# Performance work log

Hardware: AMD Instinct MI355X
Metric: run time of the kernel (lower is better)

Reference implementation:

```python
import jax, jax.numpy as jnp
import numpy as np


def _ln(z, g, b):
    m = z.mean(-1, keepdims=True)
    v = ((z - m) ** 2).mean(-1, keepdims=True)
    return (z - m) * jax.lax.rsqrt(v + 1e-5) * g + b


def _pe(T, D):
    # standard sinusoidal positional encoding (T, D)
    pos = np.arange(T)[:, None]
    i = np.arange(D // 2)[None, :]
    ang = pos / np.power(10000.0, 2.0 * i / D)
    pe = np.zeros((T, D), dtype=np.float32)
    pe[:, 0::2] = np.sin(ang)
    pe[:, 1::2] = np.cos(ang)
    return jnp.asarray(pe)


def _whconv(z, Hinc, filt, W, b):
    # Wavelet hypergraph convolution: psi diag(filt) psi^{-1} Z W + b
    # psi = heat-kernel wavelet of normalized hypergraph Laplacian, 2nd-order Taylor (K=2, s=1)
    S = Hinc.shape[0]
    Dv = Hinc.sum(1) + 1e-6          # node degrees
    De = Hinc.sum(0) + 1e-6          # hyperedge degrees
    Hn = Hinc * (Dv ** -0.5)[:, None]
    A = (Hn / De[None, :]) @ Hn.T    # Dv^-1/2 H De^-1 H^T Dv^-1/2
    I = jnp.eye(S, dtype=z.dtype)
    L = I - A
    L2 = 0.5 * (L @ L)
    psi = I - L + L2                  # exp(-L) approx
    psi_inv = I + L + L2              # exp(+L) approx
    return psi @ (filt[:, None] * (psi_inv @ z)) @ W + b


def setup_inputs():
    S, T, F, D, NS, E, K = 2048, 64, 16, 256, 4, 128, 32
    key = jax.random.key(0)
    ks = iter(jax.random.split(key, 64))
    nrm = lambda shp: jax.random.normal(next(ks), shp, jnp.float32) * 0.02
    return dict(
        x=jax.random.normal(next(ks), (S, T, F), jnp.float32),
        snapshot=(jax.random.uniform(next(ks), (NS, S, E)) < 0.05).astype(jnp.float32),
        params_snapshot=jax.random.uniform(next(ks), (NS,), jnp.float32, 0.0, 0.99),
        beta=jnp.array([0.33, 0.33, 0.33], jnp.float32),
        W_emb=nrm((F, D)), b_emb=jnp.zeros((D,), jnp.float32),
        Wq=nrm((D, D)), bq=jnp.zeros((D,), jnp.float32),
        Wk=nrm((D, D)), bk=jnp.zeros((D,), jnp.float32),
        Wv=nrm((D, D)), bv=jnp.zeros((D,), jnp.float32),
        Wo=nrm((D, D)), bo=jnp.zeros((D,), jnp.float32),
        ln1_g=jnp.ones((D,), jnp.float32), ln1_b=jnp.zeros((D,), jnp.float32),
        W_int=nrm((D, D)), b_int=jnp.zeros((D,), jnp.float32),
        W_mix=nrm((2 * D, D)), b_mix=jnp.zeros((D,), jnp.float32),
        ln2_g=jnp.ones((D,), jnp.float32), ln2_b=jnp.zeros((D,), jnp.float32),
        Wt=nrm((D, D)), bt=jnp.zeros((D,), jnp.float32), vt=nrm((D,)),
        Wh1=nrm((D, D)), bh1=jnp.zeros((D,), jnp.float32), filt1=jnp.ones((S,), jnp.float32),
        Wh2=nrm((D, D)), bh2=jnp.zeros((D,), jnp.float32), filt2=jnp.ones((S,), jnp.float32),
        Wa=nrm((D, D)), Wb=nrm((D, D)), Wg=nrm((D, D)), bg=jnp.zeros((D,), jnp.float32),
        Wm1=nrm((D, D)), bm1=jnp.zeros((D,), jnp.float32),
        Wm2=nrm((D, 1)), bm2=jnp.zeros((1,), jnp.float32),
        num_edges=K,
    )


def reference(x, snapshot, params_snapshot, beta, W_emb, b_emb, Wq, bq, Wk, bk, Wv, bv,
              Wo, bo, ln1_g, ln1_b, W_int, b_int, W_mix, b_mix, ln2_g, ln2_b,
              Wt, bt, vt, Wh1, bh1, filt1, Wh2, bh2, filt2, Wa, Wb, Wg, bg,
              Wm1, bm1, Wm2, bm2, num_edges):
    S, T, _ = x.shape
    D = W_emb.shape[1]
    H = 8
    dh = D // H
    # feature embedding + positional encoding
    h = x @ W_emb + b_emb + _pe(T, D)
    # intra-stock (per-stock temporal) multi-head self-attention + residual + LN
    q = (h @ Wq + bq).reshape(S, T, H, dh)
    k = (h @ Wk + bk).reshape(S, T, H, dh)
    v = (h @ Wv + bv).reshape(S, T, H, dh)
    att = jax.nn.softmax(jnp.einsum('sqhd,skhd->shqk', q, k) / jnp.sqrt(jnp.float32(dh)), axis=-1)
    o = jnp.einsum('shqk,skhd->sqhd', att, v).reshape(S, T, D) @ Wo + bo
    h = _ln(h + o, ln1_g, ln1_b)
    # intensity function + mixing layer (Linear -> ReLU -> LayerNorm)
    intensity = jax.nn.softplus(h @ W_int + b_int)
    z = jax.nn.relu(jnp.concatenate([h, intensity], axis=-1) @ W_mix + b_mix)
    h = _ln(z, ln2_g, ln2_b)
    # temporal attention pooling: (S,T,D) -> (S,D)
    u = jnp.tanh(h @ Wt + bt)
    a = jax.nn.softmax(u @ vt, axis=-1)          # (S,T)
    xs = jnp.einsum('st,std->sd', a, h)           # (S,D)
    # per-snapshot two-layer wavelet hypergraph conv (dropout = eval identity)
    def per_snap(Hinc):
        r1 = jax.nn.leaky_relu(_whconv(xs, Hinc, filt1, Wh1, bh1), 0.1)
        return _whconv(r1, Hinc, filt2, Wh2, bh2)
    reps = jax.vmap(per_snap)(snapshot)           # (NS,S,D)
    hyper = jnp.einsum('n,nsd->sd', params_snapshot, reps)
    # dynamic graph learning: top-k learned similarity graph
    sim = (xs @ Wa) @ (xs @ Wb).T / jnp.sqrt(jnp.float32(D))
    kth = jax.lax.top_k(sim, num_edges)[0][:, -1]
    Adyn = jax.nn.softmax(jnp.where(sim >= kth[:, None], sim, -jnp.inf), axis=-1)
    dyn = jax.nn.relu(Adyn @ xs @ Wg + bg)
    # fusion ('sum' mode) + MLP head
    w = jax.nn.softmax(beta)
    fused = w[0] * xs + w[1] * dyn + w[2] * hyper
    return jax.nn.relu(fused @ Wm1 + bm1) @ Wm2 + bm2   # (S,1)
```

## Files before the change

### kernel.cpp

```cpp
#include <hip/hip_runtime.h>
#include <math.h>

#define S_ 2048
#define T_ 64
#define F_ 16
#define D_ 256
#define NS_ 4
#define E_ 128
#define H_ 8
#define SD_ (S_*D_)
#define PS 264

#define PK_ATT 0
#define PK_WO  393216
#define PK_WI  524288
#define PK_WT  655360
#define PK_WM  786432
#define PKBASE 11674112

typedef __attribute__((ext_vector_type(8))) short bf16x8;
typedef __attribute__((ext_vector_type(4))) float f32x4;

__device__ __forceinline__ float warp_sum64(float v){
  #pragma unroll
  for (int o=32;o>=1;o>>=1) v += __shfl_xor(v,o);
  return v;
}
__device__ __forceinline__ float warp_max64(float v){
  #pragma unroll
  for (int o=32;o>=1;o>>=1) v = fmaxf(v,__shfl_xor(v,o));
  return v;
}
__device__ __forceinline__ float softplus_f(float v){
  return fmaxf(v,0.f) + log1pf(__expf(-fabsf(v)));
}
__device__ __forceinline__ float tanh_f(float v){
  float t = __expf(-2.f*fabsf(v));
  float r = (1.f-t)/(1.f+t);
  return copysignf(r, v);
}
__device__ __forceinline__ void splitf(float f, short& h, short& l){
  unsigned u = __float_as_uint(f);
  unsigned hb = (u + 0x7FFFu + ((u>>16)&1u)) >> 16;
  float fl = f - __uint_as_float(hb<<16);
  unsigned v = __float_as_uint(fl);
  unsigned lb = (v + 0x7FFFu + ((v>>16)&1u)) >> 16;
  h = (short)hb; l = (short)lb;
}
__device__ __forceinline__ f32x4 mfma3(bf16x8 ah, bf16x8 al, bf16x8 bh, bf16x8 bl, f32x4 c){
  c = __builtin_amdgcn_mfma_f32_16x16x32_bf16(al, bh, c, 0,0,0);
  c = __builtin_amdgcn_mfma_f32_16x16x32_bf16(ah, bl, c, 0,0,0);
  c = __builtin_amdgcn_mfma_f32_16x16x32_bf16(ah, bh, c, 0,0,0);
  return c;
}
__device__ __forceinline__ void afrag_f32(const float* base, int stride, int rbase, int ks, int lane, bf16x8& hi, bf16x8& lo){
  const float* p = base + (rbase + (lane&15))*stride + ks + ((lane>>4)<<3);
  #pragma unroll
  for (int jj=0;jj<8;++jj){ short h,l; splitf(p[jj],h,l); hi[jj]=h; lo[jj]=l; }
}
__device__ __forceinline__ bf16x8 afrag_pk(const short* plane, int rbase, int ks, int lane){
  return *(const bf16x8*)(plane + (rbase + (lane&15))*PS + ks + ((lane>>4)<<3));
}
__device__ __forceinline__ void bfrag_pk(const unsigned* pk, int tile, int lane, bf16x8& hi, bf16x8& lo){
  const unsigned* p = pk + (((tile<<6) + lane)<<3);
  #pragma unroll
  for (int jj=0;jj<8;++jj){ unsigned u=p[jj]; hi[jj]=(short)(u & 0xffffu); lo[jj]=(short)(u>>16); }
}
__device__ __forceinline__ void store_h(short* Hh, short* Hl, int r, int c, float f){
  short h,l; splitf(f,h,l);
  Hh[r*PS+c]=h; Hl[r*PS+c]=l;
}
__device__ __forceinline__ float load_h(const short* Hh, const short* Hl, int r, int c){
  int idx=r*PS+c;
  return __uint_as_float(((unsigned)(unsigned short)Hh[idx])<<16)
       + __uint_as_float(((unsigned)(unsigned short)Hl[idx])<<16);
}

__global__ void pack_all(const float* __restrict__ Wq, const float* __restrict__ Wk,
                         const float* __restrict__ Wv, const float* __restrict__ Wo,
                         const float* __restrict__ Wint, const float* __restrict__ Wt,
                         const float* __restrict__ Wmix, short* __restrict__ pkc){
  int y = blockIdx.y;
  int i = blockIdx.x*256 + threadIdx.x;
  if (y < 3){
    const float* W = (y==0)?Wq:((y==1)?Wk:Wv);
    int jj=i&7, n=(i>>3)&15, q=(i>>7)&3, ntg=(i>>9)&15, kt=i>>13;
    float f = W[(kt*32 + q*8 + jj)*256 + (ntg*16+n)];
    short h,l; splitf(f,h,l);
    int hp = ntg>>2, ntl = ntg&3;
    int base = ((hp*8+kt)*6 + y*2)*2048;
    int local = ntl*512 + (q*16+n)*8 + jj;
    short* dst = pkc + PK_ATT;
    dst[base+local] = h;
    dst[base+2048+local] = l;
  } else {
    const float* W; short* dst; int ib = i;
    if (y==3){W=Wo;   dst=pkc+PK_WO;}
    else if (y==4){W=Wint; dst=pkc+PK_WI;}
    else if (y==5){W=Wt;   dst=pkc+PK_WT;}
    else if (y==6){W=Wmix; dst=pkc+PK_WM;}
    else          {W=Wmix; dst=pkc+PK_WM; ib = i + 65536;}
    int jj=ib&7, n=(ib>>3)&15, q=(ib>>7)&3, ntg=(ib>>9)&15, kt=ib>>13;
    float f = W[(kt*32 + q*8 + jj)*256 + (ntg*16+n)];
    short h,l; splitf(f,h,l);
    int dl = kt*16384 + ntg*512 + (q*16+n)*8 + jj;
    dst[dl] = h; dst[dl+8192] = l;
  }
}

__global__ void pe_kernel(float* __restrict__ pe){
  int i = blockIdx.x*256 + threadIdx.x;
  int t = i >> 8, d = i & 255;
  int ii = d >> 1;
  float w = __expf(-(float)ii * (logf(10000.f)/128.f));
  float ang = (float)t * w;
  pe[i] = (d & 1) ? cosf(ang) : sinf(ang);
}

__launch_bounds__(512,1)
__global__ void stageA_kernel(
    const float* __restrict__ x, const float* __restrict__ pe,
    const float* __restrict__ Wemb, const float* __restrict__ bemb,
    const float* __restrict__ bq, const float* __restrict__ bk, const float* __restrict__ bv,
    const float* __restrict__ bo,
    const float* __restrict__ ln1g, const float* __restrict__ ln1b,
    const float* __restrict__ bint,
    const float* __restrict__ bmix,
    const float* __restrict__ ln2g, const float* __restrict__ ln2b,
    const float* __restrict__ bt,
    const float* __restrict__ vt,
    const short* __restrict__ pkc,
    float* __restrict__ xs)
{
  __shared__ __attribute__((aligned(16))) short hbh[64*PS];
  __shared__ __attribute__((aligned(16))) short hbl[64*PS];
  __shared__ __attribute__((aligned(16))) char smem[85504];

  short*    wst   = (short*)smem;
  unsigned* k2f2  = (unsigned*)smem;
  unsigned* v2f2  = (unsigned*)(smem + 16384);
  float*    qb2   = (float*)(smem + 32768);
  float*    scb2  = (float*)(smem + 50176);
  float*    poolb = (float*)smem;

  const int j  = threadIdx.x;
  const int s  = blockIdx.x;
  const int w  = j >> 6;
  const int lane = j & 63;
  const int m_ = lane & 15, qd = lane >> 4;
  const int rg2 = w >> 1, par = w & 1;
  const int rbase = rg2*16;
  const int rv = w*8;
  const int c0 = lane;

  {
    float* xb = (float*)smem;
    const float* xp = x + (long)s*T_*F_;
    for (int i=j; i<T_*F_; i+=512) xb[i] = xp[i];
  }
  __syncthreads();

  {
    const float* xb = (const float*)smem;
    float acc[8][4];
    #pragma unroll
    for (int r=0;r<8;++r){acc[r][0]=0;acc[r][1]=0;acc[r][2]=0;acc[r][3]=0;}
    #pragma unroll
    for (int k=0;k<F_;++k){
      float w0=Wemb[k*D_+c0], w1=Wemb[k*D_+c0+64], w2=Wemb[k*D_+c0+128], w3=Wemb[k*D_+c0+192];
      #pragma unroll
      for (int r=0;r<8;++r){
        float hv = xb[(rv+r)*F_+k];
        acc[r][0]+=hv*w0; acc[r][1]+=hv*w1; acc[r][2]+=hv*w2; acc[r][3]+=hv*w3;
      }
    }
    float b0=bemb[c0],b1=bemb[c0+64],b2=bemb[c0+128],b3=bemb[c0+192];
    __syncthreads();
    #pragma unroll
    for (int r=0;r<8;++r){
      int t = rv+r;
      store_h(hbh,hbl,t,c0,     acc[r][0]+b0+pe[t*D_+c0]);
      store_h(hbh,hbl,t,c0+64,  acc[r][1]+b1+pe[t*D_+c0+64]);
      store_h(hbh,hbl,t,c0+128, acc[r][2]+b2+pe[t*D_+c0+128]);
      store_h(hbh,hbl,t,c0+192, acc[r][3]+b3+pe[t*D_+c0+192]);
    }
  }
  __syncthreads();

  bf16x8 AH[8], AL[8];
  #pragma unroll
  for (int kt=0;kt<8;++kt){
    AH[kt] = afrag_pk(hbh, rbase, kt*32, lane);
    AL[kt] = afrag_pk(hbl, rbase, kt*32, lane);
  }

  const float rs = 0.17677669529663687f;
  f32x4 co[8];
  #pragma unroll
  for (int t=0;t<8;++t) co[t] = (f32x4){0.f,0.f,0.f,0.f};

  for (int hp=0; hp<4; ++hp){
    f32x4 qa[2],ka[2],va[2];
    #pragma unroll
    for (int t=0;t<2;++t){
      qa[t]=(f32x4){0.f,0.f,0.f,0.f};
      ka[t]=(f32x4){0.f,0.f,0.f,0.f};
      va[t]=(f32x4){0.f,0.f,0.f,0.f};
    }
    bf16x8 pre[3];
    {
      const short* b0 = pkc + PK_ATT + (hp*8)*12288;
      #pragma unroll
      for (int r=0;r<3;++r) pre[r] = *(const bf16x8*)(b0 + (j+r*512)*8);
    }
    __syncthreads();
    for (int kt=0; kt<8; ++kt){
      short* wb = wst + (kt&1)*12288;
      #pragma unroll
      for (int r=0;r<3;++r) *(bf16x8*)(wb + (j+r*512)*8) = pre[r];
      __syncthreads();
      if (kt<7){
        const short* nb = pkc + PK_ATT + (hp*8+kt+1)*12288;
        #pragma unroll
        for (int r=0;r<3;++r) pre[r] = *(const bf16x8*)(nb + (j+r*512)*8);
      }
      bf16x8 ah = AH[kt], al = AL[kt];
      #pragma unroll
      for (int t=0;t<2;++t){
        int ntl = par*2+t;
        bf16x8 bh,bl;
        bh = *(bf16x8*)(wb +         ntl*512 + lane*8);
        bl = *(bf16x8*)(wb + 2048  + ntl*512 + lane*8);
        qa[t]=mfma3(ah,al,bh,bl,qa[t]);
        bh = *(bf16x8*)(wb + 4096  + ntl*512 + lane*8);
        bl = *(bf16x8*)(wb + 6144  + ntl*512 + lane*8);
        ka[t]=mfma3(ah,al,bh,bl,ka[t]);
        bh = *(bf16x8*)(wb + 8192  + ntl*512 + lane*8);
        bl = *(bf16x8*)(wb + 10240 + ntl*512 + lane*8);
        va[t]=mfma3(ah,al,bh,bl,va[t]);
      }
    }
    __syncthreads();
    #pragma unroll
    for (int t=0;t<2;++t){
      int ntg = par*2+t;
      #pragma unroll
      for (int r=0;r<4;++r){
        int trow = rbase + qd*4 + r;
        int pcp = ntg*16 + m_;
        int head = pcp >> 5;
        int cp = pcp & 31;
        int col = hp*64 + pcp;
        qb2[trow*68 + pcp] = (qa[t][r] + bq[col]) * rs;
        short hS,lS;
        float kv2 = ka[t][r] + bk[col];
        splitf(kv2,hS,lS);
        k2f2[head*2048 + (((trow>>4)*4 + (cp>>3))*16 + (trow&15))*8 + (cp&7)]
            = (unsigned)(unsigned short)hS | ((unsigned)(unsigned short)lS<<16);
        float vv2 = va[t][r] + bv[col];
        splitf(vv2,hS,lS);
        v2f2[head*2048 + ((((trow>>5)*2 + (cp>>4))*4 + ((trow>>3)&3))*16 + (cp&15))*8 + (trow&7)]
            = (unsigned)(unsigned short)hS | ((unsigned)(unsigned short)lS<<16);
      }
    }
    __syncthreads();
    float* scb = scb2 + par*4352;
    {
      bf16x8 ah,al;
      afrag_f32(qb2, 68, rbase, par*32, lane, ah, al);
      f32x4 sc4[4];
      #pragma unroll
      for (int nt=0;nt<4;++nt){
        bf16x8 bh,bl; bfrag_pk(k2f2 + par*2048, nt, lane, bh, bl);
        sc4[nt] = mfma3(ah,al,bh,bl,(f32x4){0.f,0.f,0.f,0.f});
      }
      #pragma unroll
      for (int r=0;r<4;++r){
        float mx = fmaxf(fmaxf(sc4[0][r],sc4[1][r]),fmaxf(sc4[2][r],sc4[3][r]));
        #pragma unroll
        for (int o=8;o>=1;o>>=1) mx = fmaxf(mx, __shfl_xor(mx,o));
        float es = 0.f;
        #pragma unroll
        for (int nt=0;nt<4;++nt){ float e=__expf(sc4[nt][r]-mx); sc4[nt][r]=e; es+=e; }
        #pragma unroll
        for (int o=8;o>=1;o>>=1) es += __shfl_xor(es,o);
        float inv = 1.f/es;
        int trow = rbase + qd*4 + r;
        #pragma unroll
        for (int nt=0;nt<4;++nt) scb[trow*68 + nt*16 + m_] = sc4[nt][r]*inv;
      }
    }
    {
      f32x4 oa[2];
      oa[0]=(f32x4){0.f,0.f,0.f,0.f}; oa[1]=(f32x4){0.f,0.f,0.f,0.f};
      #pragma unroll
      for (int kt=0;kt<2;++kt){
        bf16x8 ah2,al2; afrag_f32(scb, 68, rbase, kt*32, lane, ah2, al2);
        #pragma unroll
        for (int nt=0;nt<2;++nt){
          bf16x8 bh,bl; bfrag_pk(v2f2 + par*2048, kt*2+nt, lane, bh, bl);
          oa[nt]=mfma3(ah2,al2,bh,bl,oa[nt]);
        }
      }
      #pragma unroll
      for (int nt=0;nt<2;++nt){
        #pragma unroll
        for (int r=0;r<4;++r)
          qb2[(rbase+qd*4+r)*68 + par*32 + nt*16 + m_] = oa[nt][r];
      }
    }
    __syncthreads();
    for (int ks=0; ks<2; ++ks){
      bf16x8 ah,al; afrag_f32(qb2, 68, rbase, ks*32, lane, ah, al);
      const short* wob = pkc + PK_WO + (hp*2+ks)*16384 + lane*8;
      #pragma unroll
      for (int t=0;t<8;++t){
        int ntg = 2*t+par;
        bf16x8 bh = *(const bf16x8*)(wob + ntg*512);
        bf16x8 bl = *(const bf16x8*)(wob + 8192 + ntg*512);
        co[t]=mfma3(ah,al,bh,bl,co[t]);
      }
    }
  }

  #pragma unroll
  for (int t=0;t<8;++t){
    int cc = (2*t+par)*16+m_;
    float bov = bo[cc];
    #pragma unroll
    for (int r=0;r<4;++r){
      int row = rbase+qd*4+r;
      store_h(hbh,hbl,row,cc, load_h(hbh,hbl,row,cc) + co[t][r] + bov);
    }
  }
  __syncthreads();

  {
    float g0=ln1g[c0],g1=ln1g[c0+64],g2=ln1g[c0+128],g3=ln1g[c0+192];
    float bb0=ln1b[c0],bb1=ln1b[c0+64],bb2=ln1b[c0+128],bb3=ln1b[c0+192];
    for (int rr=0;rr<8;++rr){
      int t=rv+rr;
      float v0=load_h(hbh,hbl,t,c0),    v1=load_h(hbh,hbl,t,c0+64);
      float v2=load_h(hbh,hbl,t,c0+128),v3=load_h(hbh,hbl,t,c0+192);
      float sm=warp_sum64(v0+v1+v2+v3);
      float sq=warp_sum64(v0*v0+v1*v1+v2*v2+v3*v3);
      float mean=sm*(1.f/256.f);
      float inv=rsqrtf(fmaxf(sq*(1.f/256.f)-mean*mean,0.f)+1e-5f);
      store_h(hbh,hbl,t,c0,    (v0-mean)*inv*g0+bb0);
      store_h(hbh,hbl,t,c0+64, (v1-mean)*inv*g1+bb1);
      store_h(hbh,hbl,t,c0+128,(v2-mean)*inv*g2+bb2);
      store_h(hbh,hbl,t,c0+192,(v3-mean)*inv*g3+bb3);
    }
  }
  __syncthreads();

  auto loadB=[&](bf16x8* d, const short* base, int kt){
    const short* p = base + kt*16384 + lane*8;
    d[0]=*(const bf16x8*)(p + (2*w)*512);
    d[1]=*(const bf16x8*)(p + 8192 + (2*w)*512);
    d[2]=*(const bf16x8*)(p + (2*w+1)*512);
    d[3]=*(const bf16x8*)(p + 8192 + (2*w+1)*512);
  };
  const short* BM = pkc + PK_WM;
  const short* BI = pkc + PK_WI;
  const short* BT = pkc + PK_WT;

  f32x4 az[4][2], ai[4][2];
  #pragma unroll
  for (int rt=0;rt<4;++rt){
    az[rt][0]=(f32x4){0.f,0.f,0.f,0.f}; az[rt][1]=(f32x4){0.f,0.f,0.f,0.f};
    ai[rt][0]=(f32x4){0.f,0.f,0.f,0.f}; ai[rt][1]=(f32x4){0.f,0.f,0.f,0.f};
  }
  bf16x8 cb[4], nb[4];
  loadB(cb, BM, 0);
  for (int kt=0; kt<8; ++kt){
    if (kt<7) loadB(nb, BM, kt+1); else loadB(nb, BI, 0);
    #pragma unroll
    for (int rt=0;rt<4;++rt){
      bf16x8 ah = afrag_pk(hbh, rt*16, kt*32, lane);
      bf16x8 al = afrag_pk(hbl, rt*16, kt*32, lane);
      az[rt][0]=mfma3(ah,al,cb[0],cb[1],az[rt][0]);
      az[rt][1]=mfma3(ah,al,cb[2],cb[3],az[rt][1]);
    }
    #pragma unroll
    for (int r=0;r<4;++r) cb[r]=nb[r];
  }
  for (int kt=0; kt<8; ++kt){
    if (kt<7) loadB(nb, BI, kt+1); else loadB(nb, BM, 8);
    #pragma unroll
    for (int rt=0;rt<4;++rt){
      bf16x8 ah = afrag_pk(hbh, rt*16, kt*32, lane);
      bf16x8 al = afrag_pk(hbl, rt*16, kt*32, lane);
      ai[rt][0]=mfma3(ah,al,cb[0],cb[1],ai[rt][0]);
      ai[rt][1]=mfma3(ah,al,cb[2],cb[3],ai[rt][1]);
    }
    #pragma unroll
    for (int r=0;r<4;++r) cb[r]=nb[r];
  }
  __syncthreads();
  #pragma unroll
  for (int rt=0;rt<4;++rt){
    #pragma unroll
    for (int t=0;t<2;++t){
      int col=(2*w+t)*16+m_;
      float bb=bint[col];
      #pragma unroll
      for (int r=0;r<4;++r)
        store_h(hbh,hbl, rt*16+qd*4+r, col, softplus_f(ai[rt][t][r]+bb));
    }
  }
  __syncthreads();
  for (int kt=0; kt<8; ++kt){
    if (kt<7) loadB(nb, BM, kt+9); else loadB(nb, BT, 0);
    #pragma unroll
    for (int rt=0;rt<4;++rt){
      bf16x8 ah = afrag_pk(hbh, rt*16, kt*32, lane);
      bf16x8 al = afrag_pk(hbl, rt*16, kt*32, lane);
      az[rt][0]=mfma3(ah,al,cb[0],cb[1],az[rt][0]);
      az[rt][1]=mfma3(ah,al,cb[2],cb[3],az[rt][1]);
    }
    #pragma unroll
    for (int r=0;r<4;++r) cb[r]=nb[r];
  }
  __syncthreads();
  #pragma unroll
  for (int rt=0;rt<4;++rt){
    #pragma unroll
    for (int t=0;t<2;++t){
      int col=(2*w+t)*16+m_;
      float bb=bmix[col];
      #pragma unroll
      for (int r=0;r<4;++r)
        store_h(hbh,hbl, rt*16+qd*4+r, col, fmaxf(az[rt][t][r]+bb,0.f));
    }
  }
  __syncthreads();
  {
    float g0=ln2g[c0],g1=ln2g[c0+64],g2=ln2g[c0+128],g3=ln2g[c0+192];
    float bb0=ln2b[c0],bb1=ln2b[c0+64],bb2=ln2b[c0+128],bb3=ln2b[c0+192];
    for (int rr=0;rr<8;++rr){
      int t=rv+rr;
      float v0=load_h(hbh,hbl,t,c0),    v1=load_h(hbh,hbl,t,c0+64);
      float v2=load_h(hbh,hbl,t,c0+128),v3=load_h(hbh,hbl,t,c0+192);
      float sm=warp_sum64(v0+v1+v2+v3);
      float sq=warp_sum64(v0*v0+v1*v1+v2*v2+v3*v3);
      float mean=sm*(1.f/256.f);
      float inv=rsqrtf(fmaxf(sq*(1.f/256.f)-mean*mean,0.f)+1e-5f);
      store_h(hbh,hbl,t,c0,    (v0-mean)*inv*g0+bb0);
      store_h(hbh,hbl,t,c0+64, (v1-mean)*inv*g1+bb1);
      store_h(hbh,hbl,t,c0+128,(v2-mean)*inv*g2+bb2);
      store_h(hbh,hbl,t,c0+192,(v3-mean)*inv*g3+bb3);
    }
  }
  __syncthreads();
  {
    f32x4 at4[4][2];
    #pragma unroll
    for (int rt=0;rt<4;++rt){
      at4[rt][0]=(f32x4){0.f,0.f,0.f,0.f}; at4[rt][1]=(f32x4){0.f,0.f,0.f,0.f};
    }
    for (int kt=0; kt<8; ++kt){
      if (kt<7) loadB(nb, BT, kt+1);
      #pragma unroll
      for (int rt=0;rt<4;++rt){
        bf16x8 ah = afrag_pk(hbh, rt*16, kt*32, lane);
        bf16x8 al = afrag_pk(hbl, rt*16, kt*32, lane);
        at4[rt][0]=mfma3(ah,al,cb[0],cb[1],at4[rt][0]);
        at4[rt][1]=mfma3(ah,al,cb[2],cb[3],at4[rt][1]);
      }
      #pragma unroll
      for (int r=0;r<4;++r) cb[r]=nb[r];
    }
    #pragma unroll
    for (int rt=0;rt<4;++rt){
      #pragma unroll
      for (int r=0;r<4;++r){
        int row = rt*16+qd*4+r;
        float p = 0.f;
        #pragma unroll
        for (int t=0;t<2;++t){
          int col=(2*w+t)*16+m_;
          p += tanh_f(at4[rt][t][r]+bt[col])*vt[col];
        }
        p += __shfl_xor(p,1); p += __shfl_xor(p,2);
        p += __shfl_xor(p,4); p += __shfl_xor(p,8);
        if (m_==0) poolb[w*64+row] = p;
      }
    }
  }
  __syncthreads();
  if (j < 64){
    float v = 0.f;
    #pragma unroll
    for (int ww=0;ww<8;++ww) v += poolb[ww*64+j];
    float m = warp_max64(v);
    float e = __expf(v-m);
    float ssum = warp_sum64(e);
    poolb[512+j] = e/ssum;
  }
  __syncthreads();
  if (j < 256){
    float acc=0.f;
    #pragma unroll 8
    for (int t=0;t<T_;++t) acc += poolb[512+t]*load_h(hbh,hbl,t,j);
    xs[(long)s*D_+j] = acc;
  }
}

__global__ void hg_deg(const float* __restrict__ Hinc, float* __restrict__ Dv, float* __restrict__ De){
  const int n = blockIdx.y, s0 = blockIdx.x*64;
  const float* Hp = Hinc + (long)n*S_*E_;
  const int j = threadIdx.x;
  {
    int r = j>>2, q = j&3;
    const float* rp = Hp + (long)(s0+r)*E_ + q*32;
    float sm=0;
    #pragma unroll
    for (int e=0;e<32;++e) sm += rp[e];
    sm += __shfl_xor(sm,1); sm += __shfl_xor(sm,2);
    if (q==0) Dv[n*S_+s0+r]=sm+1e-6f;
  }
  if (j < E_){
    float cs=0;
    for (int ss=0;ss<64;++ss) cs += Hp[(long)(s0+ss)*E_+j];
    atomicAdd(&De[n*E_+j], cs);
  }
}

__global__ void hg_scale(const float* __restrict__ Hinc, const float* __restrict__ Dv,
                         const float* __restrict__ De, float* __restrict__ Hn, float* __restrict__ HnD){
  long i = (long)blockIdx.x*256+threadIdx.x;
  int n = (int)(i >> 18);
  int rem = (int)(i & 262143);
  int srow = rem >> 7;
  int e = rem & 127;
  float h = Hinc[i];
  float hn = h * rsqrtf(Dv[n*S_+srow]);
  Hn[i] = hn;
  HnD[i] = hn / (De[n*E_+e]+1e-6f);
}

__launch_bounds__(256,2)
__global__ void hg_phase1(const float* __restrict__ Hn, const float* __restrict__ M,
                          long mz, float* __restrict__ Ppart)
{
  __shared__ float hl[64*64];
  __shared__ float ml[64*64];
  const int tile = blockIdx.x, kc = blockIdx.y, n = blockIdx.z;
  const int et = tile>>2, dt2 = tile&3;
  const int j = threadIdx.x;
  const int tx = j&15, ty = j>>4;
  float acc[4][4];
  #pragma unroll
  for (int i=0;i<4;++i){acc[i][0]=0;acc[i][1]=0;acc[i][2]=0;acc[i][3]=0;}
  for (int sub=0; sub<8; ++sub){
    int s0 = kc*512 + sub*64;
    __syncthreads();
    for (int i=j*4; i<4096; i+=1024){
      int r = i>>6, c = i&63;
      *(float4*)&hl[i] = *(const float4*)&Hn[((long)n*S_ + s0 + r)*E_ + et*64 + c];
      *(float4*)&ml[i] = *(const float4*)&M[(long)n*mz + (long)(s0+r)*D_ + dt2*64 + c];
    }
    __syncthreads();
    for (int k=0;k<64;++k){
      float4 a = *(const float4*)&hl[k*64+ty*4];
      float4 b = *(const float4*)&ml[k*64+tx*4];
      acc[0][0]+=a.x*b.x; acc[0][1]+=a.x*b.y; acc[0][2]+=a.x*b.z; acc[0][3]+=a.x*b.w;
      acc[1][0]+=a.y*b.x; acc[1][1]+=a.y*b.y; acc[1][2]+=a.y*b.z; acc[1][3]+=a.y*b.w;
      acc[2][0]+=a.z*b.x; acc[2][1]+=a.z*b.y; acc[2][2]+=a.z*b.z; acc[2][3]+=a.z*b.w;
      acc[3][0]+=a.w*b.x; acc[3][1]+=a.w*b.y; acc[3][2]+=a.w*b.z; acc[3][3]+=a.w*b.w;
    }
  }
  float* Pp = Ppart + ((long)(n*4+kc)*E_ + et*64)*D_ + dt2*64;
  #pragma unroll
  for (int i=0;i<4;++i){
    float4 v = make_float4(acc[i][0],acc[i][1],acc[i][2],acc[i][3]);
    *(float4*)&Pp[(long)(ty*4+i)*D_ + tx*4] = v;
  }
}

__launch_bounds__(256,1)
__global__ void hg_phase2(const float* __restrict__ HnD, const float* __restrict__ Ppart,
                          const float* __restrict__ X1, long x1z, float c1,
                          const float* __restrict__ X2, long x2z, float c2,
                          float c3, const float* __restrict__ filt, int usefilt,
                          float* __restrict__ out)
{
  __shared__ float al[E_*68];
  __shared__ float pl[E_*68];
  const int st = blockIdx.x*64, dt = blockIdx.y*64, n = blockIdx.z;
  const int j = threadIdx.x;
  {
    const int r = j >> 2, k0 = (j&3)*32;
    const float* hp = HnD + ((long)n*S_ + st + r)*E_ + k0;
    #pragma unroll
    for (int kk=0; kk<32; kk+=4){
      float4 v = *(const float4*)&hp[kk];
      al[(k0+kk+0)*68+r]=v.x;
      al[(k0+kk+1)*68+r]=v.y;
      al[(k0+kk+2)*68+r]=v.z;
      al[(k0+kk+3)*68+r]=v.w;
    }
  }
  const long pkz = (long)E_*D_;
  for (int idx=j; idx<E_*16; idx+=256){
    int k = idx>>4, dsub = (idx&15)*4;
    long base = ((long)(n*4)*E_ + k)*D_ + dt + dsub;
    float4 a  = *(const float4*)&Ppart[base];
    float4 b1 = *(const float4*)&Ppart[base + pkz];
    float4 b2 = *(const float4*)&Ppart[base + 2*pkz];
    float4 b3 = *(const float4*)&Ppart[base + 3*pkz];
    a.x += b1.x+b2.x+b3.x; a.y += b1.y+b2.y+b3.y;
    a.z += b1.z+b2.z+b3.z; a.w += b1.w+b2.w+b3.w;
    *(float4*)&pl[k*68+dsub] = a;
  }
  __syncthreads();
  const int tx = j&15, ty = j>>4;
  float acc[4][4];
  #pragma unroll
  for (int i=0;i<4;++i){acc[i][0]=0;acc[i][1]=0;acc[i][2]=0;acc[i][3]=0;}
  for (int k=0;k<E_;++k){
    float4 a = *(const float4*)&al[k*68+ty*4];
    float4 b = *(const float4*)&pl[k*68+tx*4];
    acc[0][0]+=a.x*b.x; acc[0][1]+=a.x*b.y; acc[0][2]+=a.x*b.z; acc[0][3]+=a.x*b.w;
    acc[1][0]+=a.y*b.x; acc[1][1]+=a.y*b.y; acc[1][2]+=a.y*b.z; acc[1][3]+=a.y*b.w;
    acc[2][0]+=a.z*b.x; acc[2][1]+=a.z*b.y; acc[2][2]+=a.z*b.z; acc[2][3]+=a.z*b.w;
    acc[3][0]+=a.w*b.x; acc[3][1]+=a.w*b.y; acc[3][2]+=a.w*b.z; acc[3][3]+=a.w*b.w;
  }
  #pragma unroll
  for (int i=0;i<4;++i){
    int srow = st + ty*4 + i;
    float f = usefilt ? filt[srow] : 1.f;
    #pragma unroll
    for (int m=0;m<4;++m){
      int d = dt + tx*4+m;
      long li = (long)srow*D_ + d;
      float v = c3*acc[i][m];
      if (X1) v += c1*X1[x1z*n + li];
      if (X2) v += c2*X2[x2z*n + li];
      out[((long)n*S_ + srow)*D_ + d] = f*v;
    }
  }
}

__launch_bounds__(256,1)
__global__ void gemm_nn(const float* __restrict__ A, long az,
                        const float* __restrict__ B, long bz,
                        float* __restrict__ C, long cz,
                        int K, int N,
                        const float* __restrict__ bias, int act)
{
  __shared__ float al[32*68];
  __shared__ float bl[32*68];
  const int mt = blockIdx.x*64, nt = blockIdx.y*64, zz = blockIdx.z;
  const int j = threadIdx.x;
  const float* Ap = A + (long)az*zz;
  const float* Bp = B + (long)bz*zz;
  const int tx = j&15, ty = j>>4;
  float acc[4][4];
  #pragma unroll
  for (int i=0;i<4;++i){acc[i][0]=0;acc[i][1]=0;acc[i][2]=0;acc[i][3]=0;}
  for (int k0=0;k0<K;k0+=32){
    #pragma unroll
    for (int half=0; half<2; ++half){
      int idx = j + half*256;
      int r = idx>>3, kk=(idx&7)*4;
      float4 v = *(const float4*)&Ap[(long)(mt+r)*K + k0+kk];
      al[(kk+0)*68+r]=v.x; al[(kk+1)*68+r]=v.y; al[(kk+2)*68+r]=v.z; al[(kk+3)*68+r]=v.w;
    }
    #pragma unroll
    for (int half=0; half<2; ++half){
      int idx = j + half*256;
      int r = idx>>4, cc=(idx&15)*4;
      *(float4*)&bl[r*68+cc] = *(const float4*)&Bp[(long)(k0+r)*N + nt+cc];
    }
    __syncthreads();
    #pragma unroll
    for (int kk=0;kk<32;++kk){
      float4 a = *(const float4*)&al[kk*68+ty*4];
      float4 b = *(const float4*)&bl[kk*68+tx*4];
      acc[0][0]+=a.x*b.x; acc[0][1]+=a.x*b.y; acc[0][2]+=a.x*b.z; acc[0][3]+=a.x*b.w;
      acc[1][0]+=a.y*b.x; acc[1][1]+=a.y*b.y; acc[1][2]+=a.y*b.z; acc[1][3]+=a.y*b.w;
      acc[2][0]+=a.z*b.x; acc[2][1]+=a.z*b.y; acc[2][2]+=a.z*b.z; acc[2][3]+=a.z*b.w;
      acc[3][0]+=a.w*b.x; acc[3][1]+=a.w*b.y; acc[3][2]+=a.w*b.z; acc[3][3]+=a.w*b.w;
    }
    __syncthreads();
  }
  #pragma unroll
  for (int i=0;i<4;++i){
    int row = mt+ty*4+i;
    #pragma unroll
    for (int m=0;m<4;++m){
      int col = nt+tx*4+m;
      float v = acc[i][m];
      if (bias) v += bias[col];
      if (act==1) v = fmaxf(v,0.f);
      else if (act==2) v = (v>0.f)? v : 0.1f*v;
      C[(long)cz*zz + (long)row*N + col] = v;
    }
  }
}

__launch_bounds__(256,1)
__global__ void gemm_nt_scaled(const float* __restrict__ A, const float* __restrict__ B,
                               float* __restrict__ C, int K, float scale)
{
  __shared__ float al[32*68];
  __shared__ float bl[32*68];
  const int mt = blockIdx.x*64, nt = blockIdx.y*64;
  const int j = threadIdx.x;
  const int tx = j&15, ty = j>>4;
  float acc[4][4];
  #pragma unroll
  for (int i=0;i<4;++i){acc[i][0]=0;acc[i][1]=0;acc[i][2]=0;acc[i][3]=0;}
  for (int k0=0;k0<K;k0+=32){
    #pragma unroll
    for (int half=0; half<2; ++half){
      int idx = j + half*256;
      int r = idx>>3, kk=(idx&7)*4;
      float4 v = *(const float4*)&A[(long)(mt+r)*K + k0+kk];
      al[(kk+0)*68+r]=v.x; al[(kk+1)*68+r]=v.y; al[(kk+2)*68+r]=v.z; al[(kk+3)*68+r]=v.w;
    }
    #pragma unroll
    for (int half=0; half<2; ++half){
      int idx = j + half*256;
      int r = idx>>3, kk=(idx&7)*4;
      float4 v = *(const float4*)&B[(long)(nt+r)*K + k0+kk];
      bl[(kk+0)*68+r]=v.x; bl[(kk+1)*68+r]=v.y; bl[(kk+2)*68+r]=v.z; bl[(kk+3)*68+r]=v.w;
    }
    __syncthreads();
    #pragma unroll
    for (int kk=0;kk<32;++kk){
      float4 a = *(const float4*)&al[kk*68+ty*4];
      float4 b = *(const float4*)&bl[kk*68+tx*4];
      acc[0][0]+=a.x*b.x; acc[0][1]+=a.x*b.y; acc[0][2]+=a.x*b.z; acc[0][3]+=a.x*b.w;
      acc[1][0]+=a.y*b.x; acc[1][1]+=a.y*b.y; acc[1][2]+=a.y*b.z; acc[1][3]+=a.y*b.w;
      acc[2][0]+=a.z*b.x; acc[2][1]+=a.z*b.y; acc[2][2]+=a.z*b.z; acc[2][3]+=a.z*b.w;
      acc[3][0]+=a.w*b.x; acc[3][1]+=a.w*b.y; acc[3][2]+=a.w*b.z; acc[3][3]+=a.w*b.w;
    }
    __syncthreads();
  }
  #pragma unroll
  for (int i=0;i<4;++i){
    #pragma unroll
    for (int m=0;m<4;++m){
      C[(long)(mt+ty*4+i)*S_ + nt+tx*4+m] = acc[i][m]*scale;
    }
  }
}

__launch_bounds__(256,4)
__global__ void topk_gather(const float* __restrict__ sim, const float* __restrict__ xs,
                            const int* __restrict__ Kp, float* __restrict__ dynpre)
{
  __shared__ float wred[4]; __shared__ int ired[4];
  __shared__ float selw[256]; __shared__ int seli[256];
  __shared__ int cnt; __shared__ float sh_kth, sh_max, sh_den; __shared__ int sh_bi;
  const int s = blockIdx.x, j = threadIdx.x;
  const float* rp = sim + (long)s*S_;
  float vo[8], v[8];
  *(float4*)&vo[0] = *(const float4*)&rp[j*8];
  *(float4*)&vo[4] = *(const float4*)&rp[j*8+4];
  #pragma unroll
  for (int r=0;r<8;++r) v[r]=vo[r];
  if (j==0) cnt=0;
  const int K = Kp[0];
  for (int it=0; it<K; ++it){
    float m=-3.0e38f; int mi=0;
    #pragma unroll
    for (int r=0;r<8;++r){ if (v[r]>m){m=v[r]; mi=r;} }
    mi += j*8;
    #pragma unroll
    for (int o=32;o>=1;o>>=1){
      float om=__shfl_xor(m,o); int oi=__shfl_xor(mi,o);
      if (om>m){m=om;mi=oi;}
    }
    if ((j&63)==0){ wred[j>>6]=m; ired[j>>6]=mi; }
    __syncthreads();
    if (j==0){
      float bm=wred[0]; int bi=ired[0];
      #pragma unroll
      for (int w=1;w<4;++w) if (wred[w]>bm){bm=wred[w];bi=ired[w];}
      sh_kth=bm; sh_bi=bi;
      if (it==0) sh_max=bm;
    }
    __syncthreads();
    int sel = sh_bi - j*8;
    #pragma unroll
    for (int r=0;r<8;++r) if (r==sel) v[r] = -3.0e38f;
  }
  const float kth=sh_kth, rmax=sh_max;
  #pragma unroll
  for (int r=0;r<8;++r){
    if (vo[r]>=kth){
      int p=atomicAdd(&cnt,1);
      if (p<256){ seli[p]=j*8+r; selw[p]=__expf(vo[r]-rmax); }
    }
  }
  __syncthreads();
  int c = cnt; if (c>256) c=256;
  {
    float p = (j<c)? selw[j] : 0.f;
    p = warp_sum64(p);
    if ((j&63)==0) wred[j>>6]=p;
    __syncthreads();
    if (j==0) sh_den = wred[0]+wred[1]+wred[2]+wred[3];
    __syncthreads();
  }
  float acc=0.f;
  for (int l=0;l<c;++l) acc += selw[l]*xs[(long)seli[l]*D_ + j];
  dynpre[(long)s*D_+j] = acc / sh_den;
}

__global__ void hyperwsum_kernel(const float* __restrict__ reps, const float* __restrict__ ps,
                                 float* __restrict__ hyper)
{
  long idx = (long)blockIdx.x*256+threadIdx.x;
  hyper[idx] = ps[0]*reps[idx] + ps[1]*reps[(long)SD_+idx]
             + ps[2]*reps[2L*SD_+idx] + ps[3]*reps[3L*SD_+idx];
}

__global__ void fuse_kernel(const float* __restrict__ xs, const float* __restrict__ dyn,
                            const float* __restrict__ hyper, const float* __restrict__ beta,
                            float* __restrict__ fused)
{
  long idx = (long)blockIdx.x*256+threadIdx.x;
  float b0=beta[0],b1=beta[1],b2=beta[2];
  float mx=fmaxf(b0,fmaxf(b1,b2));
  float e0=__expf(b0-mx),e1=__expf(b1-mx),e2=__expf(b2-mx);
  float inv=1.f/(e0+e1+e2);
  fused[idx] = e0*inv*xs[idx] + e1*inv*dyn[idx] + e2*inv*hyper[idx];
}

__global__ void head_kernel(const float* __restrict__ hh1, const float* __restrict__ Wm2,
                            const float* __restrict__ bm2, float* __restrict__ out)
{
  int r = blockIdx.x*32 + (threadIdx.x>>3);
  int sub = threadIdx.x&7;
  const float* hp = hh1 + (long)r*D_;
  float acc=0.f;
  for (int c=sub;c<D_;c+=8) acc += hp[c]*Wm2[c];
  acc += __shfl_xor(acc,1); acc += __shfl_xor(acc,2); acc += __shfl_xor(acc,4);
  if (sub==0) out[r]=acc+bm2[0];
}

extern "C" void kernel_launch(void* const* d_in, const int* in_sizes, int n_in,
                              void* d_out, int out_size, void* d_ws, size_t ws_size,
                              hipStream_t stream)
{
  (void)in_sizes;(void)n_in;(void)out_size;(void)ws_size;
  const float* x        =(const float*)d_in[0];
  const float* snapshot =(const float*)d_in[1];
  const float* ps       =(const float*)d_in[2];
  const float* beta     =(const float*)d_in[3];
  const float* Wemb=(const float*)d_in[4];  const float* bemb=(const float*)d_in[5];
  const float* Wq  =(const float*)d_in[6];  const float* bq  =(const float*)d_in[7];
  const float* Wk  =(const float*)d_in[8];  const float* bk  =(const float*)d_in[9];
  const float* Wv  =(const float*)d_in[10]; const float* bv  =(const float*)d_in[11];
  const float* Wo  =(const float*)d_in[12]; const float* bo  =(const float*)d_in[13];
  const float* ln1g=(const float*)d_in[14]; const float* ln1b=(const float*)d_in[15];
  const float* Wint=(const float*)d_in[16]; const float* bint=(const float*)d_in[17];
  const float* Wmix=(const float*)d_in[18]; const float* bmix=(const float*)d_in[19];
  const float* ln2g=(const float*)d_in[20]; const float* ln2b=(const float*)d_in[21];
  const float* Wt  =(const float*)d_in[22]; const float* bt  =(const float*)d_in[23];
  const float* vt  =(const float*)d_in[24];
  const float* Wh1 =(const float*)d_in[25]; const float* bh1 =(const float*)d_in[26];
  const float* filt1=(const float*)d_in[27];
  const float* Wh2 =(const float*)d_in[28]; const float* bh2 =(const float*)d_in[29];
  const float* filt2=(const float*)d_in[30];
  const float* Wa  =(const float*)d_in[31]; const float* Wb  =(const float*)d_in[32];
  const float* Wg  =(const float*)d_in[33]; const float* bg  =(const float*)d_in[34];
  const float* Wm1 =(const float*)d_in[35]; const float* bm1 =(const float*)d_in[36];
  const float* Wm2 =(const float*)d_in[37]; const float* bm2 =(const float*)d_in[38];
  const int* numedges=(const int*)d_in[39];
  float* out=(float*)d_out;

  float* w = (float*)d_ws;
  float* Ppart = w;
  float* Hn    = w + 4194304;
  float* HnD   = Hn + 1048576;
  float* Dv    = HnD + 1048576;
  float* De    = Dv + 8192;
  float* pe    = w;
  float* repsb = w;
  float* sim   = w;
  float* xs    = w + 6431232;
  float* hyper = xs + SD_;
  float* bufA  = hyper + SD_;
  float* bufB  = bufA + 4*SD_;
  float* p1    = bufA;
  float* q1    = bufA + SD_;
  float* dynpre= bufA + 2*SD_;
  float* dyn   = bufA + 3*SD_;
  float* fused = bufB;
  float* hh1   = bufB + SD_;
  short* pkc   = (short*)(w + PKBASE);

  hipMemsetAsync(De, 0, (size_t)NS_*E_*sizeof(float), stream);
  pe_kernel<<<64,256,0,stream>>>(pe);
  pack_all<<<dim3(256,8),256,0,stream>>>(Wq,Wk,Wv,Wo,Wint,Wt,Wmix,pkc);

  stageA_kernel<<<S_,512,0,stream>>>(x,pe,Wemb,bemb,bq,bk,bv,bo,
                                     ln1g,ln1b,bint,bmix,ln2g,ln2b,bt,vt,
                                     pkc,xs);
  hg_deg<<<dim3(32,NS_),256,0,stream>>>(snapshot,Dv,De);
  hg_scale<<<4096,256,0,stream>>>(snapshot,Dv,De,Hn,HnD);

  auto applyA=[&](const float* M, long mz,
                  const float* X1, long x1z, float c1,
                  const float* X2, long x2z, float c2, float c3,
                  const float* filt, int uf, float* outb){
    hg_phase1<<<dim3(8,4,NS_),256,0,stream>>>(Hn,M,mz,Ppart);
    hg_phase2<<<dim3(32,4,NS_),256,0,stream>>>(HnD,Ppart,X1,x1z,c1,X2,x2z,c2,c3,filt,uf,outb);
  };

  applyA(xs,0,     xs,0,1.f,    nullptr,0,0.f,  -1.f,  nullptr,0, bufA);
  applyA(bufA,SD_, xs,0,1.f,    bufA,SD_,1.5f,  -0.5f, filt1,1,   bufB);
  applyA(bufB,SD_, bufB,SD_,1.f, nullptr,0,0.f, -1.f,  nullptr,0, bufA);
  applyA(bufA,SD_, bufB,SD_,1.f, bufA,SD_,-0.5f,-0.5f, nullptr,0, bufA);
  gemm_nn<<<dim3(32,4,NS_),256,0,stream>>>(bufA,SD_, Wh1,0, bufB,SD_, 256,256, bh1, 2);

  applyA(bufB,SD_, bufB,SD_,1.f, nullptr,0,0.f, -1.f,  nullptr,0, bufA);
  applyA(bufA,SD_, bufB,SD_,1.f, bufA,SD_,1.5f, -0.5f, filt2,1,   bufB);
  applyA(bufB,SD_, bufB,SD_,1.f, nullptr,0,0.f, -1.f,  nullptr,0, bufA);
  applyA(bufA,SD_, bufB,SD_,1.f, bufA,SD_,-0.5f,-0.5f, nullptr,0, bufA);
  gemm_nn<<<dim3(32,4,NS_),256,0,stream>>>(bufA,SD_, Wh2,0, repsb,SD_, 256,256, bh2, 0);
  hyperwsum_kernel<<<2048,256,0,stream>>>(repsb,ps,hyper);

  gemm_nn<<<dim3(32,4,1),256,0,stream>>>(xs,0, Wa,0, p1,0, 256,256, nullptr, 0);
  gemm_nn<<<dim3(32,4,1),256,0,stream>>>(xs,0, Wb,0, q1,0, 256,256, nullptr, 0);
  gemm_nt_scaled<<<dim3(32,32),256,0,stream>>>(p1,q1,sim,256,0.0625f);
  topk_gather<<<S_,256,0,stream>>>(sim,xs,numedges,dynpre);
  gemm_nn<<<dim3(32,4,1),256,0,stream>>>(dynpre,0, Wg,0, dyn,0, 256,256, bg, 1);

  fuse_kernel<<<2048,256,0,stream>>>(xs,dyn,hyper,beta,fused);
  gemm_nn<<<dim3(32,4,1),256,0,stream>>>(fused,0, Wm1,0, hh1,0, 256,256, bm1, 1);
  head_kernel<<<64,256,0,stream>>>(hh1,Wm2,bm2,out);
}
```

Measured before the change: 1.632 ms.

## Replace dense hypergraph incidence GEMMs with sparse CSR gather kernels

Builds per-hyperedge and per-node compressed sparse lists from the 0/1 incidence matrix, with the degree normalisations folded into the stored values. The two dense tiled fp32 GEMM phases of each hypergraph propagation step become gather-accumulate kernels that touch only the nonzeros, avoiding the dense 2048x128 work. The lists are capped at 256 nodes per edge and 32 edges per node, so results would be silently truncated for denser incidence matrices. Separately, the attention weight staging in the first stage drops LDS double buffering in favour of a single buffer with an extra barrier per step.

```diff
diff --git a/kernel.cpp b/kernel.cpp
--- a/kernel.cpp
+++ b/kernel.cpp
@@ -213,11 +213,10 @@
       #pragma unroll
       for (int r=0;r<3;++r) pre[r] = *(const bf16x8*)(b0 + (j+r*512)*8);
     }
-    __syncthreads();
     for (int kt=0; kt<8; ++kt){
-      short* wb = wst + (kt&1)*12288;
-      #pragma unroll
-      for (int r=0;r<3;++r) *(bf16x8*)(wb + (j+r*512)*8) = pre[r];
+      __syncthreads();
+      #pragma unroll
+      for (int r=0;r<3;++r) *(bf16x8*)(wst + (j+r*512)*8) = pre[r];
       __syncthreads();
       if (kt<7){
         const short* nb = pkc + PK_ATT + (hp*8+kt+1)*12288;
@@ -229,14 +228,14 @@
       for (int t=0;t<2;++t){
         int ntl = par*2+t;
         bf16x8 bh,bl;
-        bh = *(bf16x8*)(wb +         ntl*512 + lane*8);
-        bl = *(bf16x8*)(wb + 2048  + ntl*512 + lane*8);
+        bh = *(bf16x8*)(wst +         ntl*512 + lane*8);
+        bl = *(bf16x8*)(wst + 2048  + ntl*512 + lane*8);
         qa[t]=mfma3(ah,al,bh,bl,qa[t]);
-        bh = *(bf16x8*)(wb + 4096  + ntl*512 + lane*8);
-        bl = *(bf16x8*)(wb + 6144  + ntl*512 + lane*8);
+        bh = *(bf16x8*)(wst + 4096  + ntl*512 + lane*8);
+        bl = *(bf16x8*)(wst + 6144  + ntl*512 + lane*8);
         ka[t]=mfma3(ah,al,bh,bl,ka[t]);
-        bh = *(bf16x8*)(wb + 8192  + ntl*512 + lane*8);
-        bl = *(bf16x8*)(wb + 10240 + ntl*512 + lane*8);
+        bh = *(bf16x8*)(wst + 8192  + ntl*512 + lane*8);
+        bl = *(bf16x8*)(wst + 10240 + ntl*512 + lane*8);
         va[t]=mfma3(ah,al,bh,bl,va[t]);
       }
     }
@@ -527,119 +526,80 @@
   }
 }
 
-__global__ void hg_scale(const float* __restrict__ Hinc, const float* __restrict__ Dv,
-                         const float* __restrict__ De, float* __restrict__ Hn, float* __restrict__ HnD){
-  long i = (long)blockIdx.x*256+threadIdx.x;
-  int n = (int)(i >> 18);
-  int rem = (int)(i & 262143);
-  int srow = rem >> 7;
-  int e = rem & 127;
-  float h = Hinc[i];
-  float hn = h * rsqrtf(Dv[n*S_+srow]);
-  Hn[i] = hn;
-  HnD[i] = hn / (De[n*E_+e]+1e-6f);
-}
-
-__launch_bounds__(256,2)
-__global__ void hg_phase1(const float* __restrict__ Hn, const float* __restrict__ M,
-                          long mz, float* __restrict__ Ppart)
-{
-  __shared__ float hl[64*64];
-  __shared__ float ml[64*64];
-  const int tile = blockIdx.x, kc = blockIdx.y, n = blockIdx.z;
-  const int et = tile>>2, dt2 = tile&3;
-  const int j = threadIdx.x;
-  const int tx = j&15, ty = j>>4;
-  float acc[4][4];
-  #pragma unroll
-  for (int i=0;i<4;++i){acc[i][0]=0;acc[i][1]=0;acc[i][2]=0;acc[i][3]=0;}
-  for (int sub=0; sub<8; ++sub){
-    int s0 = kc*512 + sub*64;
-    __syncthreads();
-    for (int i=j*4; i<4096; i+=1024){
-      int r = i>>6, c = i&63;
-      *(float4*)&hl[i] = *(const float4*)&Hn[((long)n*S_ + s0 + r)*E_ + et*64 + c];
-      *(float4*)&ml[i] = *(const float4*)&M[(long)n*mz + (long)(s0+r)*D_ + dt2*64 + c];
-    }
-    __syncthreads();
-    for (int k=0;k<64;++k){
-      float4 a = *(const float4*)&hl[k*64+ty*4];
-      float4 b = *(const float4*)&ml[k*64+tx*4];
-      acc[0][0]+=a.x*b.x; acc[0][1]+=a.x*b.y; acc[0][2]+=a.x*b.z; acc[0][3]+=a.x*b.w;
-      acc[1][0]+=a.y*b.x; acc[1][1]+=a.y*b.y; acc[1][2]+=a.y*b.z; acc[1][3]+=a.y*b.w;
-      acc[2][0]+=a.z*b.x; acc[2][1]+=a.z*b.y; acc[2][2]+=a.z*b.z; acc[2][3]+=a.z*b.w;
-      acc[3][0]+=a.w*b.x; acc[3][1]+=a.w*b.y; acc[3][2]+=a.w*b.z; acc[3][3]+=a.w*b.w;
-    }
-  }
-  float* Pp = Ppart + ((long)(n*4+kc)*E_ + et*64)*D_ + dt2*64;
-  #pragma unroll
-  for (int i=0;i<4;++i){
-    float4 v = make_float4(acc[i][0],acc[i][1],acc[i][2],acc[i][3]);
-    *(float4*)&Pp[(long)(ty*4+i)*D_ + tx*4] = v;
-  }
-}
-
-__launch_bounds__(256,1)
-__global__ void hg_phase2(const float* __restrict__ HnD, const float* __restrict__ Ppart,
-                          const float* __restrict__ X1, long x1z, float c1,
-                          const float* __restrict__ X2, long x2z, float c2,
-                          float c3, const float* __restrict__ filt, int usefilt,
-                          float* __restrict__ out)
-{
-  __shared__ float al[E_*68];
-  __shared__ float pl[E_*68];
-  const int st = blockIdx.x*64, dt = blockIdx.y*64, n = blockIdx.z;
-  const int j = threadIdx.x;
-  {
-    const int r = j >> 2, k0 = (j&3)*32;
-    const float* hp = HnD + ((long)n*S_ + st + r)*E_ + k0;
-    #pragma unroll
-    for (int kk=0; kk<32; kk+=4){
-      float4 v = *(const float4*)&hp[kk];
-      al[(k0+kk+0)*68+r]=v.x;
-      al[(k0+kk+1)*68+r]=v.y;
-      al[(k0+kk+2)*68+r]=v.z;
-      al[(k0+kk+3)*68+r]=v.w;
-    }
-  }
-  const long pkz = (long)E_*D_;
-  for (int idx=j; idx<E_*16; idx+=256){
-    int k = idx>>4, dsub = (idx&15)*4;
-    long base = ((long)(n*4)*E_ + k)*D_ + dt + dsub;
-    float4 a  = *(const float4*)&Ppart[base];
-    float4 b1 = *(const float4*)&Ppart[base + pkz];
-    float4 b2 = *(const float4*)&Ppart[base + 2*pkz];
-    float4 b3 = *(const float4*)&Ppart[base + 3*pkz];
-    a.x += b1.x+b2.x+b3.x; a.y += b1.y+b2.y+b3.y;
-    a.z += b1.z+b2.z+b3.z; a.w += b1.w+b2.w+b3.w;
-    *(float4*)&pl[k*68+dsub] = a;
-  }
-  __syncthreads();
-  const int tx = j&15, ty = j>>4;
-  float acc[4][4];
-  #pragma unroll
-  for (int i=0;i<4;++i){acc[i][0]=0;acc[i][1]=0;acc[i][2]=0;acc[i][3]=0;}
-  for (int k=0;k<E_;++k){
-    float4 a = *(const float4*)&al[k*68+ty*4];
-    float4 b = *(const float4*)&pl[k*68+tx*4];
-    acc[0][0]+=a.x*b.x; acc[0][1]+=a.x*b.y; acc[0][2]+=a.x*b.z; acc[0][3]+=a.x*b.w;
-    acc[1][0]+=a.y*b.x; acc[1][1]+=a.y*b.y; acc[1][2]+=a.y*b.z; acc[1][3]+=a.y*b.w;
-    acc[2][0]+=a.z*b.x; acc[2][1]+=a.z*b.y; acc[2][2]+=a.z*b.z; acc[2][3]+=a.z*b.w;
-    acc[3][0]+=a.w*b.x; acc[3][1]+=a.w*b.y; acc[3][2]+=a.w*b.z; acc[3][3]+=a.w*b.w;
-  }
-  #pragma unroll
-  for (int i=0;i<4;++i){
-    int srow = st + ty*4 + i;
-    float f = usefilt ? filt[srow] : 1.f;
-    #pragma unroll
-    for (int m=0;m<4;++m){
-      int d = dt + tx*4+m;
-      long li = (long)srow*D_ + d;
-      float v = c3*acc[i][m];
-      if (X1) v += c1*X1[x1z*n + li];
-      if (X2) v += c2*X2[x2z*n + li];
-      out[((long)n*S_ + srow)*D_ + d] = f*v;
-    }
+__global__ void build_ecsr(const float* __restrict__ snap, const float* __restrict__ Dv,
+                           int* __restrict__ ei, float* __restrict__ ev, int* __restrict__ ecnt){
+  __shared__ int cnts[257];
+  const int e = blockIdx.x, n = blockIdx.y, t = threadIdx.x;
+  const float* col = snap + (long)n*S_*E_ + e;
+  int loc[8]; int c=0;
+  #pragma unroll
+  for (int r=0;r<8;++r){
+    int s = t*8+r;
+    if (col[(long)s*E_] != 0.f) loc[c++]=s;
+  }
+  cnts[t+1]=c;
+  __syncthreads();
+  if (t==0){ cnts[0]=0; for (int i=1;i<=256;++i) cnts[i]+=cnts[i-1]; }
+  __syncthreads();
+  int base = cnts[t];
+  long eb = ((long)n*E_+e)*256;
+  for (int k=0;k<c;++k){
+    int pos = base+k;
+    if (pos<256){ ei[eb+pos]=loc[k]; ev[eb+pos]=rsqrtf(Dv[n*S_+loc[k]]); }
+  }
+  if (t==255) ecnt[n*E_+e] = min(cnts[256],256);
+}
+__global__ void build_scsr(const float* __restrict__ snap, const float* __restrict__ Dv,
+                           const float* __restrict__ De,
+                           int* __restrict__ si, float* __restrict__ sv, int* __restrict__ scnt){
+  const int s = blockIdx.x*256+threadIdx.x, n = blockIdx.y;
+  const float* row = snap + ((long)n*S_+s)*E_;
+  float vs = rsqrtf(Dv[n*S_+s]);
+  long sb = ((long)n*S_+s)*32;
+  int c=0;
+  for (int e=0;e<E_;++e){
+    if (row[e]!=0.f && c<32){
+      si[sb+c]=e;
+      sv[sb+c]=vs/(De[n*E_+e]+1e-6f);
+      ++c;
+    }
+  }
+  scnt[n*S_+s]=c;
+}
+
+__launch_bounds__(256,4)
+__global__ void hg_p1(const int* __restrict__ ei, const float* __restrict__ ev,
+                      const int* __restrict__ ecnt,
+                      const float* __restrict__ M, long mz, float* __restrict__ P){
+  const int e = blockIdx.x, n = blockIdx.y, d = threadIdx.x;
+  long eb = ((long)n*E_+e)*256;
+  const int c = ecnt[n*E_+e];
+  const float* Mp = M + (long)n*mz;
+  float acc=0.f;
+  for (int i=0;i<c;++i)
+    acc += ev[eb+i]*Mp[(long)ei[eb+i]*D_+d];
+  P[((long)n*E_+e)*D_+d]=acc;
+}
+__launch_bounds__(256,4)
+__global__ void hg_p2(const int* __restrict__ si, const float* __restrict__ sv,
+                      const int* __restrict__ scnt, const float* __restrict__ P,
+                      const float* __restrict__ X1, long x1z, float c1,
+                      const float* __restrict__ X2, long x2z, float c2,
+                      float c3, const float* __restrict__ filt, int usefilt,
+                      float* __restrict__ out){
+  const int s0 = blockIdx.x*8, n = blockIdx.y, d = threadIdx.x;
+  const float* Pn = P + (long)n*E_*D_;
+  for (int k=0;k<8;++k){
+    int s = s0+k;
+    long sb = ((long)n*S_+s)*32;
+    int c = scnt[n*S_+s];
+    float acc=0.f;
+    for (int i=0;i<c;++i) acc += sv[sb+i]*Pn[(long)si[sb+i]*D_+d];
+    long li=(long)s*D_+d;
+    float v=c3*acc;
+    if (X1) v+=c1*X1[x1z*n+li];
+    if (X2) v+=c2*X2[x2z*n+li];
+    out[((long)n*S_+s)*D_+d]=(usefilt?filt[s]:1.f)*v;
   }
 }
 
@@ -876,14 +836,18 @@
   float* out=(float*)d_out;
 
   float* w = (float*)d_ws;
-  float* Ppart = w;
-  float* Hn    = w + 4194304;
-  float* HnD   = Hn + 1048576;
-  float* Dv    = HnD + 1048576;
-  float* De    = Dv + 8192;
   float* pe    = w;
   float* repsb = w;
   float* sim   = w;
+  float* P     = w + 4194304;
+  float* Dv    = P + 131072;
+  float* De    = Dv + 8192;
+  int*   ecnt  = (int*)(De + 512);
+  int*   scnt  = ecnt + 512;
+  int*   ei    = scnt + 8192;
+  float* ev    = (float*)(ei + 131072);
+  int*   si    = (int*)(ev + 131072);
+  float* sv    = (float*)(si + 262144);
   float* xs    = w + 6431232;
   float* hyper = xs + SD_;
   float* bufA  = hyper + SD_;
@@ -904,14 +868,15 @@
                                      ln1g,ln1b,bint,bmix,ln2g,ln2b,bt,vt,
                                      pkc,xs);
   hg_deg<<<dim3(32,NS_),256,0,stream>>>(snapshot,Dv,De);
-  hg_scale<<<4096,256,0,stream>>>(snapshot,Dv,De,Hn,HnD);
+  build_ecsr<<<dim3(E_,NS_),256,0,stream>>>(snapshot,Dv,ei,ev,ecnt);
+  build_scsr<<<dim3(8,NS_),256,0,stream>>>(snapshot,Dv,De,si,sv,scnt);
 
   auto applyA=[&](const float* M, long mz,
                   const float* X1, long x1z, float c1,
                   const float* X2, long x2z, float c2, float c3,
                   const float* filt, int uf, float* outb){
-    hg_phase1<<<dim3(8,4,NS_),256,0,stream>>>(Hn,M,mz,Ppart);
-    hg_phase2<<<dim3(32,4,NS_),256,0,stream>>>(HnD,Ppart,X1,x1z,c1,X2,x2z,c2,c3,filt,uf,outb);
+    hg_p1<<<dim3(E_,NS_),256,0,stream>>>(ei,ev,ecnt,M,mz,P);
+    hg_p2<<<dim3(S_/8,NS_),256,0,stream>>>(si,sv,scnt,P,X1,x1z,c1,X2,x2z,c2,c3,filt,uf,outb);
   };
 
   applyA(xs,0,     xs,0,1.f,    nullptr,0,0.f,  -1.f,  nullptr,0, bufA);
```

After: 1.700 ms. 1.04x slower.
